# Optimization experiments

Measured on AMD Instinct MI355X. Metric: run time of the kernel, lower is better.

Reference implementation:

```python
import jax, jax.numpy as jnp
import numpy as np

N_NODES = 100000
N_EDGES = 3200000
IN_F = 128
OUT_F = 64
HEADS = 8
ALPHA = 0.2  # LeakyReLU negative slope


def setup_inputs() -> dict:
    key = jax.random.key(0)
    k1, k2, k3, k4 = jax.random.split(key, 4)
    x = jax.random.normal(k1, (N_NODES, IN_F), dtype=jnp.float32)
    edges = jax.random.randint(k2, (2, N_EDGES), 0, N_NODES, dtype=jnp.int64)
    # glorot-uniform-ish scaled params, stacked over heads
    lim_W = np.sqrt(6.0 / (IN_F + OUT_F))
    lim_a = np.sqrt(6.0 / (2 * OUT_F + 1))
    W = jax.random.uniform(k3, (HEADS, IN_F, OUT_F), minval=-lim_W, maxval=lim_W, dtype=jnp.float32)
    a = jax.random.uniform(k4, (HEADS, 2 * OUT_F, 1), minval=-lim_a, maxval=lim_a, dtype=jnp.float32)
    return {"x": x, "edges": edges, "W": W, "a": a}


def reference(x, edges, W, a):
    # x: [N, in_f]; edges: [2, E]; W: [H, in_f, out_f]; a: [H, 2*out_f, 1]
    N = x.shape[0]
    src, tgt = edges[0], edges[1]
    outs = []
    for h in range(W.shape[0]):  # small fixed head count; keeps peak memory per-head
        Wh = x @ W[h]                                  # [N, F]
        # Whij @ a == Wh[src] @ a[:F] + Wh[tgt] @ a[F:], computed at node level
        a_src = Wh @ a[h, :OUT_F, 0]                   # [N]
        a_tgt = Wh @ a[h, OUT_F:, 0]                   # [N]
        e = -jax.nn.leaky_relu(a_src[src] + a_tgt[tgt], negative_slope=ALPHA)  # [E]
        e_exp = jnp.exp(e - jnp.max(e))                # global max, as in the torch code
        denom = jax.ops.segment_sum(e_exp, src, num_segments=N) + 1e-10  # [N]
        att = e_exp / denom[src]                       # [E] edge softmax over source groups
        msg = att[:, None] * Wh[tgt]                   # [E, F]
        outs.append(jax.ops.segment_sum(msg, src, num_segments=N))  # [N, F]
    return jnp.concatenate(outs, axis=1)               # concat reduction -> [N, H*F]
```

## Files before the change

### kernel.cpp

```cpp
#include <hip/hip_runtime.h>
#include <hip/hip_bf16.h>

#define N_NODES 100000
#define N_EDGES 3200000
#define IN_F 128
#define OUT_F 64
#define HEADS 8
#define ALPHA 0.2f

#define BSHIFT 7
#define NBUCK 782
#define CHUNK 16384
#define NPBLK 196

typedef __bf16 bf16x8 __attribute__((ext_vector_type(8)));
typedef float f32x4 __attribute__((ext_vector_type(4)));
typedef __attribute__((ext_vector_type(8))) unsigned short ushort8;

static __device__ __forceinline__ unsigned short f2b(float f) {
    __hip_bfloat16 h = __float2bfloat16(f);
    return __builtin_bit_cast(unsigned short, h);
}

static __device__ __forceinline__ void gll16(const void* g, void* l) {
    __builtin_amdgcn_global_load_lds(
        (const __attribute__((address_space(1))) void*)g,
        (__attribute__((address_space(3))) void*)l, 16, 0, 0);
}

__global__ __launch_bounds__(256) void k_prep(const float* __restrict__ W,
                                              const float* __restrict__ a,
                                              unsigned short* __restrict__ Wt,
                                              float* __restrict__ u,
                                              float* __restrict__ v,
                                              int* __restrict__ bhist) {
    int b = blockIdx.x, t = threadIdx.x;
    if (b < 256) {
        int idx = b * 256 + t;
        int k = idx & 127;
        int c = idx >> 7;
        int h = c >> 6;
        int f = c & 63;
        Wt[idx] = f2b(W[h * IN_F * OUT_F + k * OUT_F + f]);
    } else if (b == 256) {
#pragma unroll
        for (int j = 0; j < 4; ++j) {
            int t2 = t + j * 256;
            int h = t2 >> 7, k = t2 & 127;
            const float* Wrow = W + h * IN_F * OUT_F + k * OUT_F;
            const float* ah = a + h * 2 * OUT_F;
            float su = 0.f, sv = 0.f;
            for (int f = 0; f < OUT_F; ++f) {
                float wv = Wrow[f];
                su += wv * ah[f];
                sv += wv * ah[OUT_F + f];
            }
            u[t2] = su;
            v[t2] = sv;
        }
    } else {
        for (int i = t; i < NBUCK; i += 256) bhist[i] = 0;
    }
}

__global__ __launch_bounds__(256) void k_xadot(const float* __restrict__ x,
                                               const float* __restrict__ u,
                                               const float* __restrict__ v,
                                               unsigned short* __restrict__ xb,
                                               float* __restrict__ asrc,
                                               float* __restrict__ atgt) {
    int node = (blockIdx.x * 256 + threadIdx.x) >> 6;
    int lane = threadIdx.x & 63;
    if (node >= N_NODES) return;
    float2 xv = *reinterpret_cast<const float2*>(x + (size_t)node * 128 + 2 * lane);
    ushort2 pv = make_ushort2(f2b(xv.x), f2b(xv.y));
    *reinterpret_cast<ushort2*>(xb + (size_t)node * 128 + 2 * lane) = pv;
    for (int h = 0; h < 8; ++h) {
        float2 uu = *reinterpret_cast<const float2*>(u + h * 128 + 2 * lane);
        float2 vv = *reinterpret_cast<const float2*>(v + h * 128 + 2 * lane);
        float s1 = xv.x * uu.x + xv.y * uu.y;
        float s2 = xv.x * vv.x + xv.y * vv.y;
        for (int d = 1; d < 64; d <<= 1) {
            s1 += __shfl_xor(s1, d);
            s2 += __shfl_xor(s2, d);
        }
        if (lane == 0) {
            asrc[node * 8 + h] = s1;
            atgt[node * 8 + h] = s2;
        }
    }
}

__global__ __launch_bounds__(256) void k_bcount(const int* __restrict__ src,
                                                int* __restrict__ bhist) {
    __shared__ int h[NBUCK];
    for (int i = threadIdx.x; i < NBUCK; i += 256) h[i] = 0;
    __syncthreads();
    int i0 = blockIdx.x * CHUNK;
    int iend = i0 + CHUNK;
    if (iend > N_EDGES) iend = N_EDGES;
    for (int i = i0 + threadIdx.x; i < iend; i += 256)
        atomicAdd(&h[src[i] >> BSHIFT], 1);
    __syncthreads();
    for (int i = threadIdx.x; i < NBUCK; i += 256)
        if (h[i]) atomicAdd(&bhist[i], h[i]);
}

__global__ __launch_bounds__(1024) void k_bscan(const int* __restrict__ bhist,
                                                int* __restrict__ bstart,
                                                int* __restrict__ bcursor,
                                                int* __restrict__ rowptr) {
    __shared__ int s[1024];
    int t = threadIdx.x;
    int v = (t < NBUCK) ? bhist[t] : 0;
    s[t] = v;
    __syncthreads();
    for (int d = 1; d < 1024; d <<= 1) {
        int add = (t >= d) ? s[t - d] : 0;
        __syncthreads();
        s[t] += add;
        __syncthreads();
    }
    if (t < NBUCK) {
        int st = s[t] - v;
        bstart[t] = st;
        bcursor[t] = st;
    }
    if (t == 0) {
        bstart[NBUCK] = N_EDGES;
        rowptr[N_NODES] = N_EDGES;
    }
}

__global__ __launch_bounds__(256) void k_bscatter(const int* __restrict__ src,
                                                  const int* __restrict__ tgt,
                                                  int* __restrict__ bcursor,
                                                  unsigned int* __restrict__ pairs) {
    __shared__ int h[NBUCK];
    __shared__ int rsv[NBUCK];
    for (int i = threadIdx.x; i < NBUCK; i += 256) h[i] = 0;
    __syncthreads();
    int i0 = blockIdx.x * CHUNK;
    int iend = i0 + CHUNK;
    if (iend > N_EDGES) iend = N_EDGES;
    for (int i = i0 + threadIdx.x; i < iend; i += 256)
        atomicAdd(&h[src[i] >> BSHIFT], 1);
    __syncthreads();
    for (int i = threadIdx.x; i < NBUCK; i += 256) {
        int c = h[i];
        rsv[i] = c ? atomicAdd(&bcursor[i], c) : 0;
        h[i] = 0;
    }
    __syncthreads();
    for (int i = i0 + threadIdx.x; i < iend; i += 256) {
        int s = src[i];
        int b = s >> BSHIFT;
        int p = rsv[b] + atomicAdd(&h[b], 1);
        pairs[p] = ((unsigned)(s & 127) << 17) | (unsigned)tgt[i];
    }
}

__global__ __launch_bounds__(256) void k_bsort(const unsigned int* __restrict__ pairs,
                                               const int* __restrict__ bstart,
                                               int* __restrict__ rowptr,
                                               int* __restrict__ stgt) {
    __shared__ int h[128];
    __shared__ int s[128];
    int b = blockIdx.x;
    int p0 = bstart[b], p1 = bstart[b + 1];
    int n0 = b << BSHIFT;
    int t = threadIdx.x;
    if (t < 128) h[t] = 0;
    __syncthreads();
    for (int i = p0 + t; i < p1; i += 256)
        atomicAdd(&h[pairs[i] >> 17], 1);
    __syncthreads();
    int v = (t < 128) ? h[t] : 0;
    if (t < 128) s[t] = v;
    __syncthreads();
    for (int d = 1; d < 128; d <<= 1) {
        int add = (t >= d && t < 128) ? s[t - d] : 0;
        __syncthreads();
        if (t < 128) s[t] += add;
        __syncthreads();
    }
    if (t < 128) {
        int pos = p0 + s[t] - v;
        int node = n0 + t;
        if (node < N_NODES) rowptr[node] = pos;
        h[t] = pos;
    }
    __syncthreads();
    for (int i = p0 + t; i < p1; i += 256) {
        unsigned int pr = pairs[i];
        int pos = atomicAdd(&h[pr >> 17], 1);
        stgt[pos] = (int)(pr & 0x1FFFF);
    }
}

__global__ __launch_bounds__(256) void k_agg10(const int* __restrict__ rowptr,
                                               const int* __restrict__ stgt,
                                               const float* __restrict__ asrc,
                                               const float* __restrict__ atgt,
                                               const unsigned short* __restrict__ xb,
                                               unsigned short* __restrict__ aggout) {
    __shared__ char lds[4 * 5120];
    const int tid = threadIdx.x;
    const int wid = tid >> 6, lane = tid & 63;
    const int node = blockIdx.x * 4 + wid;
    if (node >= N_NODES) return;
    const int seg = lane & 15;
    const int hp = lane >> 4;
    const int base = rowptr[node], end = rowptr[node + 1];
    const float2 asr = *reinterpret_cast<const float2*>(asrc + (size_t)node * 8 + hp * 2);
    char* buf = lds + wid * 5120;

    float2 accA[4] = {}, accB[4] = {};
    float den0 = 0.f, den1 = 0.f;

    const int deg = end - base;
    const int nch = (deg + 15) >> 4;

    auto eidx = [&](int c) {
        int i = base + c * 16 + seg;
        if (i >= end) i = end - 1;
        return i;
    };
    auto stage = [&](int t16) {
        int te_a = __shfl(t16, (lane & 31) >> 1);
        gll16(atgt + (size_t)te_a * 8 + (lane & 1) * 4, buf);
#pragma unroll
        for (int p = 0; p < 4; ++p) {
            int te = __shfl(t16, p * 4 + hp);
            gll16(xb + (size_t)te * 128 + seg * 8, buf + 1024 + p * 1024);
        }
    };

#define EDGE_STEP(E) { \
        uint4 xu = *reinterpret_cast<const uint4*>(Xb + (E) * 256 + seg * 16); \
        float2 w2 = *reinterpret_cast<const float2*>(buf + (E) * 32 + hp * 8); \
        _Pragma("unroll") \
        for (int i = 0; i < 4; ++i) { \
            unsigned int u = (&xu.x)[i]; \
            float2 xv; \
            xv.x = __builtin_bit_cast(float, u << 16); \
            xv.y = __builtin_bit_cast(float, u & 0xFFFF0000u); \
            asm("v_pk_fma_f32 %0, %1, %2, %0 op_sel:[0,0,0] op_sel_hi:[1,0,1]" \
                : "+v"(accA[i]) : "v"(xv), "v"(w2)); \
            asm("v_pk_fma_f32 %0, %1, %2, %0 op_sel:[0,1,0] op_sel_hi:[1,1,1]" \
                : "+v"(accB[i]) : "v"(xv), "v"(w2)); \
        } }

    if (nch > 0) {
        int t16 = stgt[eidx(0)];
        for (int c = 0; c < nch; ++c) {
            asm volatile("s_waitcnt lgkmcnt(0)" ::: "memory");
            __builtin_amdgcn_sched_barrier(0);
            stage(t16);
            if (c + 1 < nch) t16 = stgt[eidx(c + 1)];
            asm volatile("s_waitcnt vmcnt(0)" ::: "memory");
            __builtin_amdgcn_sched_barrier(0);
            int c0 = base + c * 16;
            int cnt = end - c0;
            if (cnt > 16) cnt = 16;
            {
                float2 at2 = *reinterpret_cast<const float2*>(buf + seg * 32 + hp * 8);
                float z0 = asr.x + at2.x, z1 = asr.y + at2.y;
                float e0 = (z0 > 0.f) ? -z0 : -(ALPHA * z0);
                float e1 = (z1 > 0.f) ? -z1 : -(ALPHA * z1);
                bool ok = seg < cnt;
                float w0 = ok ? __expf(e0) : 0.f;
                float w1 = ok ? __expf(e1) : 0.f;
                den0 += w0;
                den1 += w1;
                float2 wout = {w0, w1};
                *reinterpret_cast<float2*>(buf + seg * 32 + hp * 8) = wout;
            }
            asm volatile("s_waitcnt lgkmcnt(0)" ::: "memory");
            __builtin_amdgcn_sched_barrier(0);
            const char* Xb = buf + 1024;
            if (cnt == 16) {
#pragma unroll 4
                for (int e = 0; e < 16; ++e) EDGE_STEP(e)
            } else {
                for (int e = 0; e < cnt; ++e) EDGE_STEP(e)
            }
        }
    }
#undef EDGE_STEP

    for (int d = 1; d <= 8; d <<= 1) {
        den0 += __shfl_xor(den0, d);
        den1 += __shfl_xor(den1, d);
    }
    float invA = 1.f / (den0 + 1e-10f);
    float invB = 1.f / (den1 + 1e-10f);
    ushort8 oA, oB;
#pragma unroll
    for (int i = 0; i < 4; ++i) {
        oA[2 * i] = f2b(accA[i].x * invA);
        oA[2 * i + 1] = f2b(accA[i].y * invA);
        oB[2 * i] = f2b(accB[i].x * invB);
        oB[2 * i + 1] = f2b(accB[i].y * invB);
    }
    unsigned short* op = aggout + (size_t)node * 1024 + (hp * 2) * 128 + seg * 8;
    *reinterpret_cast<ushort8*>(op) = oA;
    *reinterpret_cast<ushort8*>(op + 128) = oB;
}

#define LDK2 136
__global__ __launch_bounds__(256) void k_gemm2(const unsigned short* __restrict__ agg,
                                               const unsigned short* __restrict__ Wt,
                                               float* __restrict__ out) {
    __shared__ unsigned short Al[64 * LDK2];
    __shared__ unsigned short Bl[64 * LDK2];
    const int tid = threadIdx.x;
    const int h = blockIdx.y;
    const int r0 = blockIdx.x * 64;
    for (int it = 0; it < 4; ++it) {
        int idx = tid + it * 256;
        int r = idx >> 4, k8 = (idx & 15) << 3;
        int gr = r0 + r;
        if (gr >= N_NODES) gr = N_NODES - 1;
        *reinterpret_cast<ushort8*>(&Al[r * LDK2 + k8]) =
            *reinterpret_cast<const ushort8*>(agg + (size_t)gr * 1024 + h * 128 + k8);
    }
    for (int it = 0; it < 4; ++it) {
        int idx = tid + it * 256;
        int f = idx >> 4, k8 = (idx & 15) << 3;
        *reinterpret_cast<ushort8*>(&Bl[f * LDK2 + k8]) =
            *reinterpret_cast<const ushort8*>(Wt + (size_t)(h * 64 + f) * 128 + k8);
    }
    __syncthreads();
    const int lane = tid & 63, w = tid >> 6;
    const int l15 = lane & 15, lq = lane >> 4;
    f32x4 acc[4] = {};
    for (int ks = 0; ks < 4; ++ks) {
        int koff = ks * 32 + lq * 8;
        bf16x8 af = *reinterpret_cast<const bf16x8*>(&Al[(w * 16 + l15) * LDK2 + koff]);
#pragma unroll
        for (int n = 0; n < 4; ++n) {
            bf16x8 bf_ = *reinterpret_cast<const bf16x8*>(&Bl[(n * 16 + l15) * LDK2 + koff]);
            acc[n] = __builtin_amdgcn_mfma_f32_16x16x32_bf16(af, bf_, acc[n], 0, 0, 0);
        }
    }
    for (int n = 0; n < 4; ++n) {
        int col = h * 64 + n * 16 + l15;
        int rbase = r0 + w * 16 + lq * 4;
#pragma unroll
        for (int r2 = 0; r2 < 4; ++r2) {
            int rr = rbase + r2;
            if (rr < N_NODES) out[(size_t)rr * 512 + col] = acc[n][r2];
        }
    }
}

extern "C" void kernel_launch(void* const* d_in, const int* in_sizes, int n_in,
                              void* d_out, int out_size, void* d_ws, size_t ws_size,
                              hipStream_t stream) {
    const float* x = (const float*)d_in[0];
    const int* edges = (const int*)d_in[1];
    const float* W = (const float*)d_in[2];
    const float* a = (const float*)d_in[3];
    float* out = (float*)d_out;
    const int* src = edges;
    const int* tgt = edges + N_EDGES;

    char* ws = (char*)d_ws;
    size_t off = 0;
    auto alloc = [&](size_t bytes) -> void* {
        void* p = (void*)(ws + off);
        off += (bytes + 255) & ~(size_t)255;
        return p;
    };
    unsigned short* Wt = (unsigned short*)alloc((size_t)HEADS * OUT_F * IN_F * 2);
    float* u = (float*)alloc(HEADS * IN_F * 4);
    float* v = (float*)alloc(HEADS * IN_F * 4);
    unsigned short* xb = (unsigned short*)alloc((size_t)N_NODES * IN_F * 2);
    float* asrc = (float*)alloc((size_t)N_NODES * 8 * 4);
    float* atgt = (float*)alloc((size_t)N_NODES * 8 * 4);
    int* bhist = (int*)alloc((size_t)NBUCK * 4);
    int* bstart = (int*)alloc((size_t)(NBUCK + 1) * 4);
    int* bcursor = (int*)alloc((size_t)NBUCK * 4);
    int* rowptr = (int*)alloc((size_t)(N_NODES + 1) * 4);
    unsigned int* pairs = (unsigned int*)alloc((size_t)N_EDGES * 4);
    int* stgt = (int*)alloc((size_t)N_EDGES * 4);
    (void)ws_size; (void)n_in; (void)in_sizes; (void)out_size;

    k_prep<<<258, 256, 0, stream>>>(W, a, Wt, u, v, bhist);
    k_xadot<<<25000, 256, 0, stream>>>(x, u, v, xb, asrc, atgt);
    k_bcount<<<NPBLK, 256, 0, stream>>>(src, bhist);
    k_bscan<<<1, 1024, 0, stream>>>(bhist, bstart, bcursor, rowptr);
    k_bscatter<<<NPBLK, 256, 0, stream>>>(src, tgt, bcursor, pairs);
    k_bsort<<<NBUCK, 256, 0, stream>>>(pairs, bstart, rowptr, stgt);
    k_agg10<<<25000, 256, 0, stream>>>(rowptr, stgt, asrc, atgt, xb,
                                       (unsigned short*)d_out);
    k_gemm2<<<dim3(1563, 8), 256, 0, stream>>>((const unsigned short*)d_out, Wt, out);
}
```

Measured before the change: 492.1 us.

## Fuse bucket counting into xadot, restructure attention dot, smaller sort chunks

Result: faster. 454.0 us (-7.8%).

```diff
diff --git a/kernel.cpp b/kernel.cpp
--- a/kernel.cpp
+++ b/kernel.cpp
@@ -10,8 +10,9 @@
 
 #define BSHIFT 7
 #define NBUCK 782
-#define CHUNK 16384
-#define NPBLK 196
+#define CHUNK 2048
+#define NPBLK 1563
+#define XADOT_BLKS 1024
 
 typedef __bf16 bf16x8 __attribute__((ext_vector_type(8)));
 typedef float f32x4 __attribute__((ext_vector_type(4)));
@@ -31,8 +32,7 @@
 __global__ __launch_bounds__(256) void k_prep(const float* __restrict__ W,
                                               const float* __restrict__ a,
                                               unsigned short* __restrict__ Wt,
-                                              float* __restrict__ u,
-                                              float* __restrict__ v,
+                                              float* __restrict__ uvT,
                                               int* __restrict__ bhist) {
     int b = blockIdx.x, t = threadIdx.x;
     if (b < 256) {
@@ -55,8 +55,8 @@
                 su += wv * ah[f];
                 sv += wv * ah[OUT_F + f];
             }
-            u[t2] = su;
-            v[t2] = sv;
+            uvT[k * 16 + h] = su;
+            uvT[k * 16 + 8 + h] = sv;
         }
     } else {
         for (int i = t; i < NBUCK; i += 256) bhist[i] = 0;
@@ -64,46 +64,54 @@
 }
 
 __global__ __launch_bounds__(256) void k_xadot(const float* __restrict__ x,
-                                               const float* __restrict__ u,
-                                               const float* __restrict__ v,
+                                               const float* __restrict__ uvT,
+                                               const int* __restrict__ src,
                                                unsigned short* __restrict__ xb,
                                                float* __restrict__ asrc,
-                                               float* __restrict__ atgt) {
-    int node = (blockIdx.x * 256 + threadIdx.x) >> 6;
-    int lane = threadIdx.x & 63;
-    if (node >= N_NODES) return;
-    float2 xv = *reinterpret_cast<const float2*>(x + (size_t)node * 128 + 2 * lane);
-    ushort2 pv = make_ushort2(f2b(xv.x), f2b(xv.y));
-    *reinterpret_cast<ushort2*>(xb + (size_t)node * 128 + 2 * lane) = pv;
-    for (int h = 0; h < 8; ++h) {
-        float2 uu = *reinterpret_cast<const float2*>(u + h * 128 + 2 * lane);
-        float2 vv = *reinterpret_cast<const float2*>(v + h * 128 + 2 * lane);
-        float s1 = xv.x * uu.x + xv.y * uu.y;
-        float s2 = xv.x * vv.x + xv.y * vv.y;
-        for (int d = 1; d < 64; d <<= 1) {
-            s1 += __shfl_xor(s1, d);
-            s2 += __shfl_xor(s2, d);
-        }
-        if (lane == 0) {
-            asrc[node * 8 + h] = s1;
-            atgt[node * 8 + h] = s2;
-        }
-    }
-}
-
-__global__ __launch_bounds__(256) void k_bcount(const int* __restrict__ src,
-                                                int* __restrict__ bhist) {
-    __shared__ int h[NBUCK];
-    for (int i = threadIdx.x; i < NBUCK; i += 256) h[i] = 0;
-    __syncthreads();
-    int i0 = blockIdx.x * CHUNK;
-    int iend = i0 + CHUNK;
-    if (iend > N_EDGES) iend = N_EDGES;
-    for (int i = i0 + threadIdx.x; i < iend; i += 256)
-        atomicAdd(&h[src[i] >> BSHIFT], 1);
-    __syncthreads();
-    for (int i = threadIdx.x; i < NBUCK; i += 256)
-        if (h[i]) atomicAdd(&bhist[i], h[i]);
+                                               float* __restrict__ atgt,
+                                               int* __restrict__ bhist) {
+    const int b = blockIdx.x, t = threadIdx.x;
+    if (b >= XADOT_BLKS) {
+        __shared__ int h[NBUCK];
+        for (int i = t; i < NBUCK; i += 256) h[i] = 0;
+        __syncthreads();
+        int cb = b - XADOT_BLKS;
+        int i0 = cb * CHUNK;
+        int iend = i0 + CHUNK;
+        if (iend > N_EDGES) iend = N_EDGES;
+        for (int i = i0 + t; i < iend; i += 256)
+            atomicAdd(&h[src[i] >> BSHIFT], 1);
+        __syncthreads();
+        for (int i = t; i < NBUCK; i += 256)
+            if (h[i]) atomicAdd(&bhist[i], h[i]);
+        return;
+    }
+    const int lane = t & 63, wid = t >> 6;
+    const int o = lane & 15, q = lane >> 4;
+    float up[32];
+#pragma unroll
+    for (int j = 0; j < 32; ++j) up[j] = uvT[(q * 32 + j) * 16 + o];
+
+    for (int n = b * 4 + wid; n < N_NODES; n += XADOT_BLKS * 4) {
+        const float* xr = x + (size_t)n * 128;
+        float2 xv2 = *reinterpret_cast<const float2*>(xr + 2 * lane);
+        ushort2 pv = make_ushort2(f2b(xv2.x), f2b(xv2.y));
+        *reinterpret_cast<ushort2*>(xb + (size_t)n * 128 + 2 * lane) = pv;
+        float r = 0.f;
+        const float4* xq = reinterpret_cast<const float4*>(xr + q * 32);
+#pragma unroll
+        for (int j = 0; j < 8; ++j) {
+            float4 xv = xq[j];
+            r = fmaf(xv.x, up[4 * j], r);
+            r = fmaf(xv.y, up[4 * j + 1], r);
+            r = fmaf(xv.z, up[4 * j + 2], r);
+            r = fmaf(xv.w, up[4 * j + 3], r);
+        }
+        r += __shfl_xor(r, 16);
+        r += __shfl_xor(r, 32);
+        if (lane < 8) asrc[n * 8 + o] = r;
+        else if (lane < 16) atgt[n * 8 + (o - 8)] = r;
+    }
 }
 
 __global__ __launch_bounds__(1024) void k_bscan(const int* __restrict__ bhist,
@@ -160,7 +168,7 @@
     }
 }
 
-__global__ __launch_bounds__(256) void k_bsort(const unsigned int* __restrict__ pairs,
+__global__ __launch_bounds__(512) void k_bsort(const unsigned int* __restrict__ pairs,
                                                const int* __restrict__ bstart,
                                                int* __restrict__ rowptr,
                                                int* __restrict__ stgt) {
@@ -172,7 +180,7 @@
     int t = threadIdx.x;
     if (t < 128) h[t] = 0;
     __syncthreads();
-    for (int i = p0 + t; i < p1; i += 256)
+    for (int i = p0 + t; i < p1; i += 512)
         atomicAdd(&h[pairs[i] >> 17], 1);
     __syncthreads();
     int v = (t < 128) ? h[t] : 0;
@@ -191,7 +199,7 @@
         h[t] = pos;
     }
     __syncthreads();
-    for (int i = p0 + t; i < p1; i += 256) {
+    for (int i = p0 + t; i < p1; i += 512) {
         unsigned int pr = pairs[i];
         int pos = atomicAdd(&h[pr >> 17], 1);
         stgt[pos] = (int)(pr & 0x1FFFF);
@@ -374,8 +382,7 @@
         return p;
     };
     unsigned short* Wt = (unsigned short*)alloc((size_t)HEADS * OUT_F * IN_F * 2);
-    float* u = (float*)alloc(HEADS * IN_F * 4);
-    float* v = (float*)alloc(HEADS * IN_F * 4);
+    float* uvT = (float*)alloc((size_t)IN_F * 16 * 4);
     unsigned short* xb = (unsigned short*)alloc((size_t)N_NODES * IN_F * 2);
     float* asrc = (float*)alloc((size_t)N_NODES * 8 * 4);
     float* atgt = (float*)alloc((size_t)N_NODES * 8 * 4);
@@ -387,12 +394,11 @@
     int* stgt = (int*)alloc((size_t)N_EDGES * 4);
     (void)ws_size; (void)n_in; (void)in_sizes; (void)out_size;
 
-    k_prep<<<258, 256, 0, stream>>>(W, a, Wt, u, v, bhist);
-    k_xadot<<<25000, 256, 0, stream>>>(x, u, v, xb, asrc, atgt);
-    k_bcount<<<NPBLK, 256, 0, stream>>>(src, bhist);
+    k_prep<<<258, 256, 0, stream>>>(W, a, Wt, uvT, bhist);
+    k_xadot<<<XADOT_BLKS + NPBLK, 256, 0, stream>>>(x, uvT, src, xb, asrc, atgt, bhist);
     k_bscan<<<1, 1024, 0, stream>>>(bhist, bstart, bcursor, rowptr);
     k_bscatter<<<NPBLK, 256, 0, stream>>>(src, tgt, bcursor, pairs);
-    k_bsort<<<NBUCK, 256, 0, stream>>>(pairs, bstart, rowptr, stgt);
+    k_bsort<<<NBUCK, 512, 0, stream>>>(pairs, bstart, rowptr, stgt);
     k_agg10<<<25000, 256, 0, stream>>>(rowptr, stgt, asrc, atgt, xb,
                                        (unsigned short*)d_out);
     k_gemm2<<<dim3(1563, 8), 256, 0, stream>>>((const unsigned short*)d_out, Wt, out);
```
